# Kernel tuning notes

Hardware: AMD Instinct MI355X
Metric: run time of the kernel (lower is better)

The kernel has to match this reference:

```python
import jax, jax.numpy as jnp
import numpy as np

D_MODEL = 1024
N_HEADS = 16
D_K = D_MODEL // N_HEADS


def setup_inputs() -> dict:
    key = jax.random.key(0)
    ks = jax.random.split(key, 5)
    B, T = 4, 2048
    scale = 1.0 / np.sqrt(D_MODEL)
    return {
        "x": jax.random.normal(ks[0], (B, T, D_MODEL), dtype=jnp.float32),
        "W_q": jax.random.normal(ks[1], (D_MODEL, D_MODEL), dtype=jnp.float32) * scale,
        "W_k": jax.random.normal(ks[2], (D_MODEL, D_MODEL), dtype=jnp.float32) * scale,
        "W_v": jax.random.normal(ks[3], (D_MODEL, D_MODEL), dtype=jnp.float32) * scale,
        "W_o": jax.random.normal(ks[4], (D_MODEL, D_MODEL), dtype=jnp.float32) * scale,
    }


def reference(x, W_q, W_k, W_v, W_o):
    B, T, C = x.shape
    # torch nn.Linear(bias=False): y = x @ W.T
    def proj(W):
        y = jnp.einsum('btc,dc->btd', x, W)
        # (B, T, H, Dk) -> (B, H, T, Dk)
        return y.reshape(B, T, N_HEADS, D_K).transpose(0, 2, 1, 3)

    Q, K, V = proj(W_q), proj(W_k), proj(W_v)
    scores = jnp.einsum('bhqd,bhkd->bhqk', Q, K) / jnp.sqrt(jnp.float32(D_K))
    # causal mask: disallow k > q
    causal = jnp.triu(jnp.ones((T, T), dtype=bool), k=1)
    scores = jnp.where(causal, -jnp.inf, scores)
    attn = jax.nn.softmax(scores, axis=-1)
    out = jnp.einsum('bhqk,bhkd->bhqd', attn, V)  # (B, H, T, Dk)
    out = out.transpose(0, 2, 1, 3).reshape(B, T, C)
    return jnp.einsum('btc,dc->btd', out, W_o)
```

## Files before the change

### kernel.cpp

```cpp
#include <hip/hip_runtime.h>

typedef unsigned short u16;
typedef __attribute__((ext_vector_type(8))) short short8;
typedef __attribute__((ext_vector_type(4))) float f32x4;
typedef __attribute__((ext_vector_type(16))) float f32x16;

__device__ __forceinline__ u16 f2bf(float f) {
    union { float f; unsigned u; } v; v.f = f;
    unsigned r = v.u + 0x7fff + ((v.u >> 16) & 1);
    return (u16)(r >> 16);
}

__device__ __forceinline__ unsigned cvtpk(float lo, float hi) {
    unsigned r;
    asm("v_cvt_pk_bf16_f32 %0, %1, %2" : "=v"(r) : "v"(lo), "v"(hi));
    return r;
}

__device__ __forceinline__ void plswap(unsigned& a, unsigned& b) {
    auto r = __builtin_amdgcn_permlane32_swap((int)a, (int)b, false, false);
    a = (unsigned)r[0]; b = (unsigned)r[1];
}

__device__ __forceinline__ void gload_lds16(const void* g, void* l) {
    __builtin_amdgcn_global_load_lds(
        (const __attribute__((address_space(1))) void*)g,
        (__attribute__((address_space(3))) void*)l, 16, 0, 0);
}

__global__ __launch_bounds__(256) void cvt_all(
    const float* __restrict__ x, const float* __restrict__ wq, const float* __restrict__ wk,
    const float* __restrict__ wv, const float* __restrict__ wo,
    u16* __restrict__ xb, u16* __restrict__ wqb, u16* __restrict__ wkb,
    u16* __restrict__ wvb, u16* __restrict__ wob)
{
    const int b = blockIdx.x;
    const float* src; u16* dst; int base;
    if (b < 8192)       { src = x;  dst = xb;  base = b; }
    else if (b < 9216)  { src = wq; dst = wqb; base = b - 8192; }
    else if (b < 10240) { src = wk; dst = wkb; base = b - 9216; }
    else if (b < 11264) { src = wv; dst = wvb; base = b - 10240; }
    else                { src = wo; dst = wob; base = b - 11264; }
    const int i = base * 256 + threadIdx.x;
    float4 v = ((const float4*)src)[i];
    ushort4 o;
    o.x = f2bf(v.x); o.y = f2bf(v.y); o.z = f2bf(v.z); o.w = f2bf(v.w);
    ((ushort4*)dst)[i] = o;
}

__global__ __launch_bounds__(256) void gemm_qkv(
    const u16* __restrict__ Agl, const u16* __restrict__ Wq, const u16* __restrict__ Wk,
    const u16* __restrict__ Wv, u16* __restrict__ Qo, u16* __restrict__ Ko, u16* __restrict__ Vo)
{
    __shared__ alignas(16) u16 As[128 * 64];
    __shared__ alignas(16) u16 Bs[128 * 64];
    const int tid = threadIdx.x;
    const int lane = tid & 63;
    const int w = tid >> 6;
    const int wr = w >> 1, wc = w & 1;
    const int bid = blockIdx.x;
    const int xcd = bid & 7;
    const int j   = bid >> 3;
    const int nb  = j & 7;
    const int rem = j >> 3;
    const int z   = rem >> 3;
    const int yb  = (xcd << 3) | (rem & 7);
    const int m0 = yb * 128;
    const int n0 = nb * 128;
    const u16* Bgl = (z == 0) ? Wq : (z == 1) ? Wk : Wv;

    f32x4 acc[4][4] = {};

    for (int kt = 0; kt < 16; ++kt) {
        const int kb = kt * 64;
#pragma unroll
        for (int p = 0; p < 4; ++p) {
            const int row = p * 32 + (tid >> 3);
            const int ke = kb + (((tid & 7) * 8) ^ ((row & 7) * 8));
            gload_lds16(Agl + (size_t)(m0 + row) * 1024 + ke, (char*)As + p * 4096 + w * 1024);
            gload_lds16(Bgl + (size_t)(n0 + row) * 1024 + ke, (char*)Bs + p * 4096 + w * 1024);
        }
        __syncthreads();
#pragma unroll
        for (int ks = 0; ks < 2; ++ks) {
            short8 a[4], b[4];
#pragma unroll
            for (int m = 0; m < 4; ++m) {
                const int row = wr * 64 + m * 16 + (lane & 15);
                const int ke = (ks * 32 + (lane >> 4) * 8) ^ ((row & 7) * 8);
                a[m] = *(const short8*)(&As[row * 64 + ke]);
            }
#pragma unroll
            for (int n = 0; n < 4; ++n) {
                const int row = wc * 64 + n * 16 + (lane & 15);
                const int ke = (ks * 32 + (lane >> 4) * 8) ^ ((row & 7) * 8);
                b[n] = *(const short8*)(&Bs[row * 64 + ke]);
            }
#pragma unroll
            for (int m = 0; m < 4; ++m)
#pragma unroll
                for (int n = 0; n < 4; ++n)
                    acc[m][n] = __builtin_amdgcn_mfma_f32_16x16x32_bf16(a[m], b[n], acc[m][n], 0, 0, 0);
        }
        __syncthreads();
    }
    const float qs = (z == 0) ? 0.18033688011112043f : 1.0f;
#pragma unroll
    for (int m = 0; m < 4; ++m)
#pragma unroll
        for (int n = 0; n < 4; ++n)
#pragma unroll
            for (int r = 0; r < 4; ++r) {
                const int row = m0 + wr * 64 + m * 16 + ((lane >> 4) << 2) + r;
                const int col = n0 + wc * 64 + n * 16 + (lane & 15);
                const u16 bv = f2bf(acc[m][n][r] * qs);
                const int bb = row >> 11, t = row & 2047, h = col >> 6, dk = col & 63;
                if (z == 2) {
                    Vo[((size_t)(bb * 16 + h) * 64 + dk) * 2048 + t] = bv;
                } else {
                    u16* dst = (z == 0) ? Qo : Ko;
                    dst[(((size_t)(bb * 16 + h) * 2048 + t) << 6) + dk] = bv;
                }
            }
}

__global__ __launch_bounds__(256) void gemm_out(
    const u16* __restrict__ Agl, const u16* __restrict__ Bgl, float* __restrict__ Co)
{
    __shared__ alignas(16) u16 As[128 * 64];
    __shared__ alignas(16) u16 Bs[128 * 64];
    const int tid = threadIdx.x;
    const int lane = tid & 63;
    const int w = tid >> 6;
    const int wr = w >> 1, wc = w & 1;
    const int bid = blockIdx.x;
    const int xcd = bid & 7;
    const int j   = bid >> 3;
    const int nb  = j & 7;
    const int yb  = (xcd << 3) | (j >> 3);
    const int m0 = yb * 128;
    const int n0 = nb * 128;

    f32x4 acc[4][4] = {};

    for (int kt = 0; kt < 16; ++kt) {
        const int kb = kt * 64;
#pragma unroll
        for (int p = 0; p < 4; ++p) {
            const int row = p * 32 + (tid >> 3);
            const int ke = kb + (((tid & 7) * 8) ^ ((row & 7) * 8));
            gload_lds16(Agl + (size_t)(m0 + row) * 1024 + ke, (char*)As + p * 4096 + w * 1024);
            gload_lds16(Bgl + (size_t)(n0 + row) * 1024 + ke, (char*)Bs + p * 4096 + w * 1024);
        }
        __syncthreads();
#pragma unroll
        for (int ks = 0; ks < 2; ++ks) {
            short8 a[4], b[4];
#pragma unroll
            for (int m = 0; m < 4; ++m) {
                const int row = wr * 64 + m * 16 + (lane & 15);
                const int ke = (ks * 32 + (lane >> 4) * 8) ^ ((row & 7) * 8);
                a[m] = *(const short8*)(&As[row * 64 + ke]);
            }
#pragma unroll
            for (int n = 0; n < 4; ++n) {
                const int row = wc * 64 + n * 16 + (lane & 15);
                const int ke = (ks * 32 + (lane >> 4) * 8) ^ ((row & 7) * 8);
                b[n] = *(const short8*)(&Bs[row * 64 + ke]);
            }
#pragma unroll
            for (int m = 0; m < 4; ++m)
#pragma unroll
                for (int n = 0; n < 4; ++n)
                    acc[m][n] = __builtin_amdgcn_mfma_f32_16x16x32_bf16(a[m], b[n], acc[m][n], 0, 0, 0);
        }
        __syncthreads();
    }
#pragma unroll
    for (int m = 0; m < 4; ++m)
#pragma unroll
        for (int n = 0; n < 4; ++n)
#pragma unroll
            for (int r = 0; r < 4; ++r) {
                const int row = m0 + wr * 64 + m * 16 + ((lane >> 4) << 2) + r;
                const int col = n0 + wc * 64 + n * 16 + (lane & 15);
                Co[(size_t)row * 1024 + col] = acc[m][n][r];
            }
}

__global__ __launch_bounds__(256, 4) void attn_fwd2(
    const u16* __restrict__ Q, const u16* __restrict__ Kg,
    const u16* __restrict__ Vt, u16* __restrict__ O)
{
    __shared__ alignas(16) u16 Ks[2][64 * 64];
    __shared__ alignas(16) u16 Vs[2][64 * 64];
    __shared__ alignas(16) float abuf[4][32];

    const int tid = threadIdx.x;
    const int lane = tid & 63;
    const int w = tid >> 6;
    const int l31 = lane & 31;
    const int hi = lane >> 5;
    const int bid = blockIdx.x;
    const int s  = bid >> 8;
    const int g  = bid & 255;
    const int u  = g >> 3;
    const int bh = ((u & 7) << 3) | (g & 7);
    const int jj = u >> 3;
    const int p  = ((s >> 1) << 2) | jj;
    const int qc = (s & 1) ? p : (15 - p);
    const size_t hb = (size_t)bh << 17;
    const int bb = bh >> 4, h = bh & 15;

    const int q0 = qc * 128;
    const int wq0 = q0 + w * 32;
    const int ntiles = qc * 2 + 2;
    const int qrow = wq0 + l31;

    short8 qf[4];
#pragma unroll
    for (int ks = 0; ks < 4; ++ks)
        qf[ks] = *(const short8*)(&Q[hb + ((size_t)qrow << 6) + ks * 16 + hi * 8]);

    f32x16 o0 = {}, o1 = {};
    float lsum = 0.f;

#pragma unroll
    for (int pp = 0; pp < 2; ++pp) {
        const int c = pp * 256 + tid;
        const int row = c >> 3;
        const int ke = ((c & 7) * 8) ^ ((row & 7) * 8);
        gload_lds16(&Kg[hb + ((size_t)row << 6) + ke], (char*)Ks[0] + pp * 4096 + w * 1024);
        gload_lds16(&Vt[hb + ((size_t)row << 11) + ke], (char*)Vs[0] + pp * 4096 + w * 1024);
    }
    __syncthreads();

    for (int t = 0; t < ntiles; ++t) {
        const int cur = t & 1;
        if (t + 1 < ntiles) {
            const int t0n = (t + 1) * 64;
#pragma unroll
            for (int pp = 0; pp < 2; ++pp) {
                const int c = pp * 256 + tid;
                const int row = c >> 3;
                const int ke = ((c & 7) * 8) ^ ((row & 7) * 8);
                gload_lds16(&Kg[hb + ((size_t)(t0n + row) << 6) + ke], (char*)Ks[cur ^ 1] + pp * 4096 + w * 1024);
                gload_lds16(&Vt[hb + ((size_t)row << 11) + t0n + ke], (char*)Vs[cur ^ 1] + pp * 4096 + w * 1024);
            }
        }
        const int t0 = t * 64;
        if (t0 <= wq0 + 31) {
            const u16* ks_ = Ks[cur];
            const u16* vs_ = Vs[cur];
            const bool full1 = (t0 + 32 <= wq0 + 31);
            f32x16 s0 = {}, s1 = {};
            __builtin_amdgcn_s_setprio(1);
#pragma unroll
            for (int ks = 0; ks < 4; ++ks) {
                const int d0 = ks * 16 + hi * 8;
                const int r0 = l31;
                short8 kf0 = *(const short8*)(&ks_[r0 * 64 + (d0 ^ ((r0 & 7) * 8))]);
                s0 = __builtin_amdgcn_mfma_f32_32x32x16_bf16(kf0, qf[ks], s0, 0, 0, 0);
            }
            if (full1) {
#pragma unroll
                for (int ks = 0; ks < 4; ++ks) {
                    const int d0 = ks * 16 + hi * 8;
                    const int r1 = 32 + l31;
                    short8 kf1 = *(const short8*)(&ks_[r1 * 64 + (d0 ^ ((r1 & 7) * 8))]);
                    s1 = __builtin_amdgcn_mfma_f32_32x32x16_bf16(kf1, qf[ks], s1, 0, 0, 0);
                }
            }
            __builtin_amdgcn_s_setprio(0);
            if (t0 + 63 > wq0) {
#pragma unroll
                for (int r = 0; r < 16; ++r) {
                    const int kva = t0 + (r & 3) + 8 * (r >> 2) + 4 * hi;
                    if (kva > qrow)                s0[r] = -1e30f;
                    if (full1 && kva + 32 > qrow)  s1[r] = -1e30f;
                }
            }
            float rs = 0.f;
            unsigned pwv[16];
            const int nsl = full1 ? 4 : 2;
#pragma unroll
            for (int sl = 0; sl < 4; ++sl) {
                if (sl >= nsl) break;
                float pv[8];
#pragma unroll
                for (int i = 0; i < 8; ++i) {
                    const float sv = (sl < 2) ? s0[(sl & 1) * 8 + i] : s1[(sl & 1) * 8 + i];
                    pv[i] = exp2f(sv);
                    rs += pv[i];
                }
                unsigned w01 = cvtpk(pv[0], pv[1]);
                unsigned w23 = cvtpk(pv[2], pv[3]);
                unsigned w45 = cvtpk(pv[4], pv[5]);
                unsigned w67 = cvtpk(pv[6], pv[7]);
                plswap(w01, w45);
                plswap(w23, w67);
                pwv[sl * 4 + 0] = w01; pwv[sl * 4 + 1] = w23;
                pwv[sl * 4 + 2] = w45; pwv[sl * 4 + 3] = w67;
            }
            rs += __shfl_xor(rs, 32);
            lsum += rs;
            __builtin_amdgcn_s_setprio(1);
#pragma unroll
            for (int sl = 0; sl < 4; ++sl) {
                if (sl >= nsl) break;
                union { unsigned uu4[4]; short8 s8; } uu;
                uu.uu4[0] = pwv[sl * 4 + 0]; uu.uu4[1] = pwv[sl * 4 + 1];
                uu.uu4[2] = pwv[sl * 4 + 2]; uu.uu4[3] = pwv[sl * 4 + 3];
                const int tc = sl * 16 + hi * 8;
                const int r0 = l31, r1 = 32 + l31;
                short8 vf0 = *(const short8*)(&vs_[r0 * 64 + (tc ^ ((r0 & 7) * 8))]);
                short8 vf1 = *(const short8*)(&vs_[r1 * 64 + (tc ^ ((r1 & 7) * 8))]);
                o0 = __builtin_amdgcn_mfma_f32_32x32x16_bf16(uu.s8, vf0, o0, 0, 0, 0);
                o1 = __builtin_amdgcn_mfma_f32_32x32x16_bf16(uu.s8, vf1, o1, 0, 0, 0);
            }
            __builtin_amdgcn_s_setprio(0);
        }
        __syncthreads();
    }
    if (hi == 0) abuf[w][l31] = __builtin_amdgcn_rcpf(lsum);
#pragma unroll
    for (int c = 0; c < 4; ++c) {
        const f32x4 a4 = *(const f32x4*)(&abuf[w][c * 8 + hi * 4]);
#pragma unroll
        for (int e = 0; e < 4; ++e) {
            const int r = c * 4 + e;
            const int qr = wq0 + (r & 3) + 8 * (r >> 2) + 4 * hi;
            const size_t rb = ((size_t)(bb * 2048 + qr) << 10) + h * 64;
            O[rb + l31]      = f2bf(o0[r] * a4[e]);
            O[rb + 32 + l31] = f2bf(o1[r] * a4[e]);
        }
    }
}

extern "C" void kernel_launch(void* const* d_in, const int* in_sizes, int n_in,
                              void* d_out, int out_size, void* d_ws, size_t ws_size,
                              hipStream_t stream) {
    const float* x  = (const float*)d_in[0];
    const float* Wq = (const float*)d_in[1];
    const float* Wk = (const float*)d_in[2];
    const float* Wv = (const float*)d_in[3];
    const float* Wo = (const float*)d_in[4];
    char* ws = (char*)d_ws;
    const size_t MB = 1u << 20;
    u16* xb   = (u16*)(ws);
    u16* Ob   = (u16*)(ws);
    u16* wqb  = (u16*)(ws + 16 * MB);
    u16* wkb  = (u16*)(ws + 18 * MB);
    u16* wvb  = (u16*)(ws + 20 * MB);
    u16* wob  = (u16*)(ws + 22 * MB);
    u16* Qws  = (u16*)(ws + 24 * MB);
    u16* Kws  = (u16*)(ws + 40 * MB);
    u16* Vtws = (u16*)(ws + 56 * MB);

    cvt_all<<<12288, 256, 0, stream>>>(x, Wq, Wk, Wv, Wo, xb, wqb, wkb, wvb, wob);
    gemm_qkv<<<1536, 256, 0, stream>>>(xb, wqb, wkb, wvb, Qws, Kws, Vtws);
    attn_fwd2<<<1024, 256, 0, stream>>>(Qws, Kws, Vtws, Ob);
    gemm_out<<<512, 256, 0, stream>>>(Ob, wob, (float*)d_out);
}
```

Measured before the change: 253.6 us.

## Double-buffer LDS tiles in QKV and output GEMMs to overlap loads with MFMA

```diff
diff --git a/kernel.cpp b/kernel.cpp
--- a/kernel.cpp
+++ b/kernel.cpp
@@ -48,12 +48,12 @@
     ((ushort4*)dst)[i] = o;
 }
 
-__global__ __launch_bounds__(256) void gemm_qkv(
+__global__ __launch_bounds__(256, 2) void gemm_qkv(
     const u16* __restrict__ Agl, const u16* __restrict__ Wq, const u16* __restrict__ Wk,
     const u16* __restrict__ Wv, u16* __restrict__ Qo, u16* __restrict__ Ko, u16* __restrict__ Vo)
 {
-    __shared__ alignas(16) u16 As[128 * 64];
-    __shared__ alignas(16) u16 Bs[128 * 64];
+    __shared__ alignas(16) u16 As[2][128 * 64];
+    __shared__ alignas(16) u16 Bs[2][128 * 64];
     const int tid = threadIdx.x;
     const int lane = tid & 63;
     const int w = tid >> 6;
@@ -71,16 +71,27 @@
 
     f32x4 acc[4][4] = {};
 
-    for (int kt = 0; kt < 16; ++kt) {
-        const int kb = kt * 64;
+    auto stage = [&](int buf, int kb) {
 #pragma unroll
         for (int p = 0; p < 4; ++p) {
             const int row = p * 32 + (tid >> 3);
             const int ke = kb + (((tid & 7) * 8) ^ ((row & 7) * 8));
-            gload_lds16(Agl + (size_t)(m0 + row) * 1024 + ke, (char*)As + p * 4096 + w * 1024);
-            gload_lds16(Bgl + (size_t)(n0 + row) * 1024 + ke, (char*)Bs + p * 4096 + w * 1024);
-        }
-        __syncthreads();
+            gload_lds16(Agl + (size_t)(m0 + row) * 1024 + ke, (char*)As[buf] + p * 4096 + w * 1024);
+            gload_lds16(Bgl + (size_t)(n0 + row) * 1024 + ke, (char*)Bs[buf] + p * 4096 + w * 1024);
+        }
+    };
+
+    stage(0, 0);
+    for (int kt = 0; kt < 16; ++kt) {
+        const int cur = kt & 1;
+        if (kt < 15) {
+            stage(cur ^ 1, (kt + 1) * 64);
+            asm volatile("s_waitcnt vmcnt(8)" ::: "memory");
+        } else {
+            asm volatile("s_waitcnt vmcnt(0)" ::: "memory");
+        }
+        __builtin_amdgcn_s_barrier();
+        asm volatile("" ::: "memory");
 #pragma unroll
         for (int ks = 0; ks < 2; ++ks) {
             short8 a[4], b[4];
@@ -88,13 +99,13 @@
             for (int m = 0; m < 4; ++m) {
                 const int row = wr * 64 + m * 16 + (lane & 15);
                 const int ke = (ks * 32 + (lane >> 4) * 8) ^ ((row & 7) * 8);
-                a[m] = *(const short8*)(&As[row * 64 + ke]);
+                a[m] = *(const short8*)(&As[cur][row * 64 + ke]);
             }
 #pragma unroll
             for (int n = 0; n < 4; ++n) {
                 const int row = wc * 64 + n * 16 + (lane & 15);
                 const int ke = (ks * 32 + (lane >> 4) * 8) ^ ((row & 7) * 8);
-                b[n] = *(const short8*)(&Bs[row * 64 + ke]);
+                b[n] = *(const short8*)(&Bs[cur][row * 64 + ke]);
             }
 #pragma unroll
             for (int m = 0; m < 4; ++m)
@@ -102,7 +113,9 @@
                 for (int n = 0; n < 4; ++n)
                     acc[m][n] = __builtin_amdgcn_mfma_f32_16x16x32_bf16(a[m], b[n], acc[m][n], 0, 0, 0);
         }
-        __syncthreads();
+        asm volatile("" ::: "memory");
+        __builtin_amdgcn_s_barrier();
+        asm volatile("" ::: "memory");
     }
     const float qs = (z == 0) ? 0.18033688011112043f : 1.0f;
 #pragma unroll
@@ -124,11 +137,11 @@
             }
 }
 
-__global__ __launch_bounds__(256) void gemm_out(
+__global__ __launch_bounds__(256, 2) void gemm_out(
     const u16* __restrict__ Agl, const u16* __restrict__ Bgl, float* __restrict__ Co)
 {
-    __shared__ alignas(16) u16 As[128 * 64];
-    __shared__ alignas(16) u16 Bs[128 * 64];
+    __shared__ alignas(16) u16 As[2][128 * 64];
+    __shared__ alignas(16) u16 Bs[2][128 * 64];
     const int tid = threadIdx.x;
     const int lane = tid & 63;
     const int w = tid >> 6;
@@ -143,16 +156,27 @@
 
     f32x4 acc[4][4] = {};
 
-    for (int kt = 0; kt < 16; ++kt) {
-        const int kb = kt * 64;
+    auto stage = [&](int buf, int kb) {
 #pragma unroll
         for (int p = 0; p < 4; ++p) {
             const int row = p * 32 + (tid >> 3);
             const int ke = kb + (((tid & 7) * 8) ^ ((row & 7) * 8));
-            gload_lds16(Agl + (size_t)(m0 + row) * 1024 + ke, (char*)As + p * 4096 + w * 1024);
-            gload_lds16(Bgl + (size_t)(n0 + row) * 1024 + ke, (char*)Bs + p * 4096 + w * 1024);
-        }
-        __syncthreads();
+            gload_lds16(Agl + (size_t)(m0 + row) * 1024 + ke, (char*)As[buf] + p * 4096 + w * 1024);
+            gload_lds16(Bgl + (size_t)(n0 + row) * 1024 + ke, (char*)Bs[buf] + p * 4096 + w * 1024);
+        }
+    };
+
+    stage(0, 0);
+    for (int kt = 0; kt < 16; ++kt) {
+        const int cur = kt & 1;
+        if (kt < 15) {
+            stage(cur ^ 1, (kt + 1) * 64);
+            asm volatile("s_waitcnt vmcnt(8)" ::: "memory");
+        } else {
+            asm volatile("s_waitcnt vmcnt(0)" ::: "memory");
+        }
+        __builtin_amdgcn_s_barrier();
+        asm volatile("" ::: "memory");
 #pragma unroll
         for (int ks = 0; ks < 2; ++ks) {
             short8 a[4], b[4];
@@ -160,13 +184,13 @@
             for (int m = 0; m < 4; ++m) {
                 const int row = wr * 64 + m * 16 + (lane & 15);
                 const int ke = (ks * 32 + (lane >> 4) * 8) ^ ((row & 7) * 8);
-                a[m] = *(const short8*)(&As[row * 64 + ke]);
+                a[m] = *(const short8*)(&As[cur][row * 64 + ke]);
             }
 #pragma unroll
             for (int n = 0; n < 4; ++n) {
                 const int row = wc * 64 + n * 16 + (lane & 15);
                 const int ke = (ks * 32 + (lane >> 4) * 8) ^ ((row & 7) * 8);
-                b[n] = *(const short8*)(&Bs[row * 64 + ke]);
+                b[n] = *(const short8*)(&Bs[cur][row * 64 + ke]);
             }
 #pragma unroll
             for (int m = 0; m < 4; ++m)
@@ -174,7 +198,9 @@
                 for (int n = 0; n < 4; ++n)
                     acc[m][n] = __builtin_amdgcn_mfma_f32_16x16x32_bf16(a[m], b[n], acc[m][n], 0, 0, 0);
         }
-        __syncthreads();
+        asm volatile("" ::: "memory");
+        __builtin_amdgcn_s_barrier();
+        asm volatile("" ::: "memory");
     }
 #pragma unroll
     for (int m = 0; m < 4; ++m)
```

New measurement: 240.3 us. -5.3%, faster.
